# Optimization experiments

Hardware: AMD Instinct MI355X
Metric: run time of the kernel (lower is better)

Reference implementation:

```python
import jax, jax.numpy as jnp
import numpy as np

N_NODES = 50000


def gcn_conv(x, src, dst, inv_sqrt_deg, W):
    # GCNConv: h = x @ W^T, then out[i] = sum_{j->i} norm_ji * h[j]
    h = x @ W.T                                   # [N, out]
    norm = inv_sqrt_deg[src] * inv_sqrt_deg[dst]  # [E]
    msg = h[src] * norm[:, None]                  # [E, out] gather
    return jax.ops.segment_sum(msg, dst, num_segments=N_NODES)  # scatter-add


def setup_inputs() -> dict:
    key = jax.random.key(0)
    k1, k2, k3, k4, k5 = jax.random.split(key, 5)
    x = jax.random.normal(k1, (N_NODES, 500), dtype=jnp.float32)
    edge_index = jax.random.randint(k2, (2, 1600000), 0, N_NODES, dtype=jnp.int64)
    W1 = jax.random.normal(k3, (128, 500), dtype=jnp.float32) * 0.04
    W2 = jax.random.normal(k4, (128, 128), dtype=jnp.float32) * 0.08
    Wlin = jax.random.normal(k5, (16, 128), dtype=jnp.float32) * 0.08
    return {"x": x, "edge_index": edge_index, "W1": W1, "W2": W2, "Wlin": Wlin}


def reference(x, edge_index, W1, W2, Wlin):
    # add self-loops (GCNConv default)
    loop = jnp.arange(N_NODES, dtype=edge_index.dtype)
    src = jnp.concatenate([edge_index[0], loop])
    dst = jnp.concatenate([edge_index[1], loop])
    # symmetric normalization: deg counted on destination (in-degree incl. self-loop)
    deg = jax.ops.segment_sum(jnp.ones_like(src, dtype=x.dtype), dst, num_segments=N_NODES)
    inv_sqrt_deg = jnp.where(deg > 0, jax.lax.rsqrt(deg), 0.0)

    h = gcn_conv(x, src, dst, inv_sqrt_deg, W1)
    h = jax.nn.relu(h)
    h = gcn_conv(h, src, dst, inv_sqrt_deg, W2)
    # dropout is identity in eval mode (training=False reference)
    return h @ Wlin.T  # [N, num_classes]
```

## Files before the change

kernel.cpp:

```cpp
#include <hip/hip_runtime.h>

#define N_NODES 50000
#define F_IN 500
#define F_HID 128
#define F_OUT 16
#define NSCAN_BLKS ((N_NODES + 255) / 256)


__device__ __forceinline__ unsigned bf16_pack2(float a, float b) {
    unsigned ua = __float_as_uint(a);
    unsigned ub = __float_as_uint(b);
    ua = (ua + 0x7fffu + ((ua >> 16) & 1u)) >> 16;
    ub = (ub + 0x7fffu + ((ub >> 16) & 1u)) >> 16;
    return ua | (ub << 16);
}
__device__ __forceinline__ float bf_lo(unsigned v) { return __uint_as_float(v << 16); }
__device__ __forceinline__ float bf_hi(unsigned v) { return __uint_as_float(v & 0xffff0000u); }

__device__ __forceinline__ unsigned bf16_rtne(float a) {
    unsigned u = __float_as_uint(a);
    return (u + 0x7fffu + ((u >> 16) & 1u)) >> 16;
}


__global__ void k_hist_rank(const int* __restrict__ dst, int* __restrict__ hist,
                            int* __restrict__ rank, int E) {
    int e = blockIdx.x * 256 + threadIdx.x;
    if (e < E) rank[e] = atomicAdd(&hist[dst[e]], 1);
}

__global__ __launch_bounds__(256) void k_scan_local(const int* __restrict__ hist,
                                                    int* __restrict__ rowptr,
                                                    int* __restrict__ blksum) {
    __shared__ int s[256];
    const int tid = threadIdx.x;
    const int i = blockIdx.x * 256 + tid;
    int v = (i < N_NODES) ? hist[i] : 0;
    s[tid] = v;
    __syncthreads();
#pragma unroll
    for (int ofs = 1; ofs < 256; ofs <<= 1) {
        int t = (tid >= ofs) ? s[tid - ofs] : 0;
        __syncthreads();
        if (tid >= ofs) s[tid] += t;
        __syncthreads();
    }
    if (i < N_NODES) rowptr[i] = s[tid] - v;
    if (tid == 255) blksum[blockIdx.x] = s[255];
}

__global__ __launch_bounds__(256) void k_scan_blk(int* __restrict__ blksum) {
    __shared__ int s[256];
    const int tid = threadIdx.x;
    int v = (tid < NSCAN_BLKS) ? blksum[tid] : 0;
    s[tid] = v;
    __syncthreads();
#pragma unroll
    for (int ofs = 1; ofs < 256; ofs <<= 1) {
        int t = (tid >= ofs) ? s[tid - ofs] : 0;
        __syncthreads();
        if (tid >= ofs) s[tid] += t;
        __syncthreads();
    }
    if (tid < NSCAN_BLKS) blksum[tid] = s[tid] - v;
}

__global__ void k_finalize(const int* __restrict__ hist, int* __restrict__ rowptr,
                           const int* __restrict__ blksum, float* __restrict__ isd, int E) {
    int i = blockIdx.x * 256 + threadIdx.x;
    if (i < N_NODES) {
        rowptr[i] = rowptr[i] + blksum[i >> 8];
        isd[i] = rsqrtf((float)(hist[i] + 1));
    }
    if (i == 0) rowptr[N_NODES] = E;
}

__global__ void k_reorder(const int* __restrict__ src, const int* __restrict__ dst,
                          const int* __restrict__ rank, const int* __restrict__ rowptr,
                          int* __restrict__ csr_src, int E) {
    int e = blockIdx.x * 256 + threadIdx.x;
    if (e >= E) return;
    csr_src[rowptr[dst[e]] + rank[e]] = src[e];
}


__global__ void k_wc(const float* __restrict__ W2, const float* __restrict__ Wlin,
                     float* __restrict__ Wc) {
    const int c = blockIdx.x;
    const int j = threadIdx.x;
    const float* wl = Wlin + c * 128;
    float acc = 0.f;
#pragma unroll 4
    for (int k = 0; k < 128; ++k) acc += wl[k] * W2[k * 128 + j];
    Wc[c * 128 + j] = acc;
}


__global__ __launch_bounds__(256) void k_w1pack(const float* __restrict__ W1,
                                                ushort* __restrict__ wpk) {
    int t = blockIdx.x * 256 + threadIdx.x;
    if (t >= 8192) return;
    const int lane = t & 63;
    const int fkt = t >> 6;
    const int f = fkt & 7;
    const int kt = fkt >> 3;
    const int n = (f << 4) + (lane & 15);
    const int kb = (kt << 5) + ((lane >> 4) << 3);
    ushort h8[8], l8[8];
#pragma unroll
    for (int j = 0; j < 8; ++j) {
        const int k = kb + j;
        float v = (k < F_IN) ? W1[n * F_IN + k] : 0.f;
        unsigned h = bf16_rtne(v);
        float fh = __uint_as_float(h << 16);
        unsigned l = bf16_rtne(v - fh);
        h8[j] = (ushort)h;
        l8[j] = (ushort)l;
    }
    const size_t base = ((size_t)fkt << 10);
    *(uint4*)(wpk + base + (lane << 3))       = *(const uint4*)h8;
    *(uint4*)(wpk + base + 512 + (lane << 3)) = *(const uint4*)l8;
}


typedef __attribute__((ext_vector_type(8))) short s16x8;
typedef __attribute__((ext_vector_type(4))) float f32x4;

typedef const __attribute__((address_space(1))) unsigned u32_glb;
typedef __attribute__((address_space(3))) unsigned u32_lds;

__device__ __forceinline__ void glds16(const void* g, void* l) {
    __builtin_amdgcn_global_load_lds((u32_glb*)g, (u32_lds*)l, 16, 0, 0);
}

__global__ __launch_bounds__(256) void gemm1_mfma5(const float* __restrict__ A,
                                                   const ushort* __restrict__ wpk,
                                                   const float* __restrict__ isd,
                                                   unsigned* __restrict__ hb, int M) {
    __shared__ __align__(16) ushort Bs[2][8192];

    const int tid = threadIdx.x;
    const int lane = tid & 63;
    const int wave = tid >> 6;
    const int jcol = lane & 15;
    const int kgrp = lane >> 4;
    const int klo  = kgrp << 3;

    const int m0  = blockIdx.x * 64 + wave * 16;
    const int arw = m0 + jcol;
    const float* arow = A + (size_t)((arw < M) ? arw : (M - 1)) * F_IN;

#define ISSUE_TILE(KT, B)                                                        \
    {                                                                            \
        const ushort* tb_ = wpk + ((size_t)(KT) << 13);                          \
        _Pragma("unroll") for (int c_ = 0; c_ < 4; ++c_) {                       \
            glds16(tb_ + ((c_ * 256 + wave * 64 + lane) << 3),                   \
                   &Bs[B][(c_ * 256 + wave * 64) << 3]);                         \
        }                                                                        \
    }

    const float4 zf4 = make_float4(0.f, 0.f, 0.f, 0.f);
    float4 ca0 = zf4, ca1 = zf4;

    ISSUE_TILE(0, 0);
    ca0 = *(const float4*)(arow + klo);
    ca1 = *(const float4*)(arow + klo + 4);
    __syncthreads();

    f32x4 acc[8] = {};

    for (int kt = 0; kt < 16; ++kt) {
        const int cb = kt & 1, nb = (kt + 1) & 1;

        float4 na0 = zf4, na1 = zf4;
        if (kt + 1 < 16) {
            ISSUE_TILE(kt + 1, nb);
            const int k = ((kt + 1) << 5) + klo;
            if (k + 8 <= F_IN) {
                na0 = *(const float4*)(arow + k);
                na1 = *(const float4*)(arow + k + 4);
            } else {
                float tmp[8];
#pragma unroll
                for (int i = 0; i < 8; ++i) tmp[i] = (k + i < F_IN) ? arow[k + i] : 0.f;
                na0 = make_float4(tmp[0], tmp[1], tmp[2], tmp[3]);
                na1 = make_float4(tmp[4], tmp[5], tmp[6], tmp[7]);
            }
        }

        const float av[8] = {ca0.x, ca0.y, ca0.z, ca0.w, ca1.x, ca1.y, ca1.z, ca1.w};
        s16x8 ahi, alo;
#pragma unroll
        for (int i = 0; i < 8; ++i) {
            unsigned h = bf16_rtne(av[i]);
            float fh = __uint_as_float(h << 16);
            unsigned l = bf16_rtne(av[i] - fh);
            ahi[i] = (short)h;
            alo[i] = (short)l;
        }

#pragma unroll
        for (int f = 0; f < 8; ++f) {
            const s16x8 bh = *(const s16x8*)&Bs[cb][(f << 10) + (lane << 3)];
            const s16x8 bl = *(const s16x8*)&Bs[cb][(f << 10) + 512 + (lane << 3)];
            acc[f] = __builtin_amdgcn_mfma_f32_16x16x32_bf16(ahi, bh, acc[f], 0, 0, 0);
            acc[f] = __builtin_amdgcn_mfma_f32_16x16x32_bf16(alo, bh, acc[f], 0, 0, 0);
            acc[f] = __builtin_amdgcn_mfma_f32_16x16x32_bf16(ahi, bl, acc[f], 0, 0, 0);
        }

        ca0 = na0;
        ca1 = na1;
        __syncthreads();
    }
#undef ISSUE_TILE

    const int orow = m0 + (kgrp << 2);
    float sr[4];
#pragma unroll
    for (int r = 0; r < 4; ++r) {
        const int m = orow + r;
        sr[r] = (m < M) ? isd[m] : 0.f;
    }
#pragma unroll
    for (int f = 0; f < 8; ++f) {
#pragma unroll
        for (int r = 0; r < 4; ++r) {
            float v = acc[f][r] * sr[r];
            float o = __shfl_xor(v, 1, 64);
            if (!(jcol & 1)) {
                const int m = orow + r;
                if (m < M)
                    hb[(size_t)m * 64 + (f << 3) + (jcol >> 1)] = bf16_pack2(v, o);
            }
        }
    }
}


__device__ __forceinline__ void gather_range(const unsigned* __restrict__ hh,
                                             const int* __restrict__ csr_src,
                                             int lane, int e, int end,
                                             float& accx, float& accy) {
    int s[8], t[8];
    bool have = (e + 8 <= end);
    if (have) {
#pragma unroll
        for (int i = 0; i < 8; ++i) s[i] = csr_src[e + i];
    }
    while (have) {
        unsigned v[8];
#pragma unroll
        for (int i = 0; i < 8; ++i) v[i] = hh[(size_t)s[i] * 64 + lane];
        const int ne = e + 8;
        const bool nhave = (ne + 8 <= end);
        if (nhave) {
#pragma unroll
            for (int i = 0; i < 8; ++i) t[i] = csr_src[ne + i];
        }
#pragma unroll
        for (int i = 0; i < 8; ++i) {
            accx += bf_lo(v[i]);
            accy += bf_hi(v[i]);
        }
#pragma unroll
        for (int i = 0; i < 8; ++i) s[i] = t[i];
        e = ne;
        have = nhave;
    }
    if (e < end) {
        const int last = end - 1;
        int ss[8];
        unsigned vv[8];
#pragma unroll
        for (int i = 0; i < 8; ++i) ss[i] = csr_src[(e + i < end) ? e + i : last];
#pragma unroll
        for (int i = 0; i < 8; ++i) vv[i] = hh[(size_t)ss[i] * 64 + lane];
#pragma unroll
        for (int i = 0; i < 8; ++i) {
            if (e + i < end) {
                accx += bf_lo(vv[i]);
                accy += bf_hi(vv[i]);
            }
        }
    }
}

__global__ __launch_bounds__(256) void k_gather_fused2(const unsigned* __restrict__ hh,
                                                       const int* __restrict__ rowptr,
                                                       const int* __restrict__ csr_src,
                                                       const float* __restrict__ isd,
                                                       const float* __restrict__ Wc,
                                                       float* __restrict__ z) {
    __shared__ float2 part[2][64];
    const int tid = threadIdx.x;
    const int lane = tid & 63;
    const int waveid = tid >> 6;
    const int slot = waveid >> 1;
    const int half = waveid & 1;
    const int node = (blockIdx.x << 1) + slot;

    const int e0 = rowptr[node], e1 = rowptr[node + 1];
    const int mid = e0 + ((e1 - e0) >> 1);

    float accx = 0.f, accy = 0.f;
    if (half == 0) {
        const unsigned a = hh[(size_t)node * 64 + lane];
        accx = bf_lo(a);
        accy = bf_hi(a);
        gather_range(hh, csr_src, lane, e0, mid, accx, accy);
    } else {
        gather_range(hh, csr_src, lane, mid, e1, accx, accy);
        part[slot][lane] = make_float2(accx, accy);
    }
    __syncthreads();
    if (half == 1) return;

    const float2 pb = part[slot][lane];
    accx += pb.x;
    accy += pb.y;

    const float si = isd[node];
    const float rx = fmaxf(accx * si, 0.f), ry = fmaxf(accy * si, 0.f);
    float p[16];
#pragma unroll
    for (int c = 0; c < 16; ++c) {
        const float2 wc = *(const float2*)(Wc + c * 128 + (lane << 1));
        p[c] = rx * wc.x + ry * wc.y;
    }
#pragma unroll
    for (int m = 1; m < 64; m <<= 1) {
#pragma unroll
        for (int c = 0; c < 16; ++c) p[c] += __shfl_xor(p[c], m, 64);
    }
    if (lane == 0) {
        float* zr = z + (size_t)node * 16;
        *(float4*)(zr + 0)  = make_float4(si * p[0],  si * p[1],  si * p[2],  si * p[3]);
        *(float4*)(zr + 4)  = make_float4(si * p[4],  si * p[5],  si * p[6],  si * p[7]);
        *(float4*)(zr + 8)  = make_float4(si * p[8],  si * p[9],  si * p[10], si * p[11]);
        *(float4*)(zr + 12) = make_float4(si * p[12], si * p[13], si * p[14], si * p[15]);
    }
}


__global__ __launch_bounds__(256) void k_gather16(const float4* __restrict__ z4,
                                                  const int* __restrict__ rowptr,
                                                  const int* __restrict__ csr_src,
                                                  const float* __restrict__ isd,
                                                  float4* __restrict__ out4) {
    int t = blockIdx.x * 256 + threadIdx.x;
    int n = t >> 2, q = t & 3;
    if (n >= N_NODES) return;
    const float si = isd[n];
    float4 acc = z4[(size_t)n * 4 + q];
    int e = rowptr[n];
    const int end = rowptr[n + 1];
    for (; e + 4 <= end; e += 4) {
        int s0 = csr_src[e],     s1 = csr_src[e + 1];
        int s2 = csr_src[e + 2], s3 = csr_src[e + 3];
        float4 v0 = z4[(size_t)s0 * 4 + q];
        float4 v1 = z4[(size_t)s1 * 4 + q];
        float4 v2 = z4[(size_t)s2 * 4 + q];
        float4 v3 = z4[(size_t)s3 * 4 + q];
        acc.x += v0.x + v1.x + v2.x + v3.x;
        acc.y += v0.y + v1.y + v2.y + v3.y;
        acc.z += v0.z + v1.z + v2.z + v3.z;
        acc.w += v0.w + v1.w + v2.w + v3.w;
    }
    for (; e < end; ++e) {
        int s = csr_src[e];
        float4 v = z4[(size_t)s * 4 + q];
        acc.x += v.x; acc.y += v.y; acc.z += v.z; acc.w += v.w;
    }
    acc.x *= si; acc.y *= si; acc.z *= si; acc.w *= si;
    out4[(size_t)n * 4 + q] = acc;
}


__global__ void k_deg_init(float* __restrict__ deg) {
    int i = blockIdx.x * 256 + threadIdx.x;
    if (i < N_NODES) deg[i] = 1.0f;
}
__global__ void k_deg_count(const int* __restrict__ dst, float* __restrict__ deg, int E) {
    int e = blockIdx.x * 256 + threadIdx.x;
    if (e < E) atomicAdd(&deg[dst[e]], 1.0f);
}
__global__ void k_rsqrt(float* __restrict__ deg) {
    int i = blockIdx.x * 256 + threadIdx.x;
    if (i < N_NODES) deg[i] = rsqrtf(deg[i]);
}
__global__ void k_agg_init(const float4* __restrict__ h, const float* __restrict__ isd,
                           float4* __restrict__ agg) {
    int t = blockIdx.x * 256 + threadIdx.x;
    if (t < N_NODES * (F_HID / 4)) {
        int row = t >> 5;
        float s = isd[row];
        s = s * s;
        float4 v = h[t];
        v.x *= s; v.y *= s; v.z *= s; v.w *= s;
        agg[t] = v;
    }
}
__global__ void k_scatter(const float4* __restrict__ h, const int* __restrict__ src,
                          const int* __restrict__ dst, const float* __restrict__ isd,
                          float* __restrict__ agg, int E) {
    int t = blockIdx.x * 256 + threadIdx.x;
    int e = t >> 5, q = t & 31;
    if (e >= E) return;
    int s = src[e], d = dst[e];
    float norm = isd[s] * isd[d];
    float4 v = h[(long long)s * 32 + q];
    float* out = agg + (long long)d * F_HID + q * 4;
    atomicAdd(out + 0, v.x * norm);
    atomicAdd(out + 1, v.y * norm);
    atomicAdd(out + 2, v.z * norm);
    atomicAdd(out + 3, v.w * norm);
}
template <int BM, int BN, int BK, int TM, int TN, bool RELU_A>
__global__ __launch_bounds__(256) void gemm_nt(const float* __restrict__ A,
                                               const float* __restrict__ B,
                                               float* __restrict__ C,
                                               int M, int N, int K) {
    __shared__ float As[BK][BM + 1];
    __shared__ float Bs[BK][BN + 1];
    const int tid = threadIdx.x;
    const int NTX = BN / TN;
    const int tx = tid % NTX;
    const int ty = tid / NTX;
    const int m0 = blockIdx.x * BM;
    const int n0 = blockIdx.y * BN;
    float acc[TM][TN] = {};
    for (int k0 = 0; k0 < K; k0 += BK) {
        for (int idx = tid; idx < BM * BK; idx += 256) {
            int m = idx / BK, k = idx % BK;
            int gm = m0 + m;
            float v = (gm < M) ? A[(long long)gm * K + k0 + k] : 0.0f;
            if (RELU_A) v = fmaxf(v, 0.0f);
            As[k][m] = v;
        }
        for (int idx = tid; idx < BN * BK; idx += 256) {
            int n = idx / BK, k = idx % BK;
            int gn = n0 + n;
            Bs[k][n] = (gn < N) ? B[(long long)gn * K + k0 + k] : 0.0f;
        }
        __syncthreads();
        for (int k = 0; k < BK; ++k) {
            float a[TM], b[TN];
#pragma unroll
            for (int r = 0; r < TM; ++r) a[r] = As[k][ty * TM + r];
#pragma unroll
            for (int c = 0; c < TN; ++c) b[c] = Bs[k][c * NTX + tx];
#pragma unroll
            for (int r = 0; r < TM; ++r)
#pragma unroll
                for (int c = 0; c < TN; ++c) acc[r][c] += a[r] * b[c];
        }
        __syncthreads();
    }
#pragma unroll
    for (int r = 0; r < TM; ++r) {
        int gm = m0 + ty * TM + r;
        if (gm >= M) continue;
#pragma unroll
        for (int c = 0; c < TN; ++c) {
            int gn = n0 + c * NTX + tx;
            if (gn < N) C[(long long)gm * N + gn] = acc[r][c];
        }
    }
}
__global__ __launch_bounds__(256) void gemm_lin(const float* __restrict__ A,
                                                const float* __restrict__ W,
                                                float* __restrict__ C, int M) {
    __shared__ float Ws[16][129];
    __shared__ float As[16][129];
    const int tid = threadIdx.x;
    for (int idx = tid; idx < 16 * 128; idx += 256) Ws[idx >> 7][idx & 127] = W[idx];
    const int m0 = blockIdx.x * 16;
    for (int idx = tid; idx < 16 * 128; idx += 256) {
        int r = idx >> 7, k = idx & 127;
        int gm = m0 + r;
        As[r][k] = (gm < M) ? A[(long long)gm * 128 + k] : 0.0f;
    }
    __syncthreads();
    const int tc = tid & 15, tr = tid >> 4;
    float s = 0.f;
#pragma unroll 8
    for (int k = 0; k < 128; ++k) s += As[tr][k] * Ws[tc][k];
    int gm = m0 + tr;
    if (gm < M) C[gm * 16 + tc] = s;
}


static inline size_t align256(size_t x) { return (x + 255) & ~(size_t)255; }

extern "C" void kernel_launch(void* const* d_in, const int* in_sizes, int n_in,
                              void* d_out, int out_size, void* d_ws, size_t ws_size,
                              hipStream_t stream) {
    const float* x    = (const float*)d_in[0];
    const int*   ei   = (const int*)d_in[1];
    const float* W1   = (const float*)d_in[2];
    const float* W2   = (const float*)d_in[3];
    const float* Wlin = (const float*)d_in[4];
    float* out = (float*)d_out;

    const int E = in_sizes[1] / 2;
    const int* src = ei;
    const int* dst = ei + E;

    char* ws = (char*)d_ws;
    size_t off = 0;
    float* isd  = (float*)(ws + off); off += align256((size_t)N_NODES * 4);
    float* Wc   = (float*)(ws + off); off += align256(16 * 128 * 4);
    float* bufA = (float*)(ws + off); off += align256((size_t)N_NODES * F_HID * 4);
    float* bufB = (float*)(ws + off); off += align256((size_t)N_NODES * F_HID * 4);
    int*   hist    = (int*)(ws + off); off += align256((size_t)N_NODES * 4);
    int*   rowptr  = (int*)(ws + off); off += align256(((size_t)N_NODES + 1) * 4);
    int*   blksum  = (int*)(ws + off); off += align256(256 * 4);
    int*   csr_src = (int*)(ws + off); off += align256((size_t)E * 4);
    int*   rank    = (int*)(ws + off); off += align256((size_t)E * 4);
    ushort* wpk    = (ushort*)(ws + off); off += align256((size_t)16 * 8192 * 2);
    const bool use_csr = (off <= ws_size);

    const int nblk_nodes = NSCAN_BLKS;
    const int nblk_edges = (E + 255) / 256;
    const int mtiles = (N_NODES + 63) / 64;

    if (use_csr) {
        unsigned* hb = (unsigned*)bufB;
        float*    z  = bufA;

        hipMemsetAsync(hist, 0, (size_t)N_NODES * 4, stream);
        k_hist_rank<<<nblk_edges, 256, 0, stream>>>(dst, hist, rank, E);
        k_scan_local<<<nblk_nodes, 256, 0, stream>>>(hist, rowptr, blksum);
        k_scan_blk<<<1, 256, 0, stream>>>(blksum);
        k_finalize<<<nblk_nodes, 256, 0, stream>>>(hist, rowptr, blksum, isd, E);
        k_reorder<<<nblk_edges, 256, 0, stream>>>(src, dst, rank, rowptr, csr_src, E);
        k_wc<<<16, 128, 0, stream>>>(W2, Wlin, Wc);
        k_w1pack<<<32, 256, 0, stream>>>(W1, wpk);
        gemm1_mfma5<<<mtiles, 256, 0, stream>>>(x, wpk, isd, hb, N_NODES);
        k_gather_fused2<<<N_NODES / 2, 256, 0, stream>>>(
            hb, rowptr, csr_src, isd, Wc, z);
        k_gather16<<<(N_NODES * 4 + 255) / 256, 256, 0, stream>>>(
            (const float4*)z, rowptr, csr_src, isd, (float4*)out);
    } else {
        const int nblk_feat = (N_NODES * (F_HID / 4) + 255) / 256;
        const int nblk_scatter = (int)(((long long)E * 32 + 255) / 256);
        k_deg_init<<<(N_NODES + 255) / 256, 256, 0, stream>>>(isd);
        k_deg_count<<<nblk_edges, 256, 0, stream>>>(dst, isd, E);
        k_rsqrt<<<(N_NODES + 255) / 256, 256, 0, stream>>>(isd);
        gemm_nt<64, 128, 20, 4, 8, false>
            <<<dim3(mtiles, 1), 256, 0, stream>>>(x, W1, bufA, N_NODES, F_HID, F_IN);
        k_agg_init<<<nblk_feat, 256, 0, stream>>>((const float4*)bufA, isd, (float4*)bufB);
        k_scatter<<<nblk_scatter, 256, 0, stream>>>((const float4*)bufA, src, dst, isd, bufB, E);
        gemm_nt<64, 128, 16, 4, 8, true>
            <<<dim3(mtiles, 1), 256, 0, stream>>>(bufB, W2, bufA, N_NODES, F_HID, F_HID);
        k_agg_init<<<nblk_feat, 256, 0, stream>>>((const float4*)bufA, isd, (float4*)bufB);
        k_scatter<<<nblk_scatter, 256, 0, stream>>>((const float4*)bufA, src, dst, isd, bufB, E);
        gemm_lin<<<(N_NODES + 15) / 16, 256, 0, stream>>>(bufB, Wlin, out, N_NODES);
    }
}
```

Baseline: 405.1 us.

## Gather two edges per wave with 8-byte loads and split output projection across waves

The layer-2 gather now has each half-wave read a different neighbour row using 8-byte uint2 loads, so one wave covers two edges per load instruction. The half-wave partial sums are combined with a cross-half shuffle. The final 16-column projection, which the first wave used to do alone, is split so each of the two waves computes 8 output columns with float4 weight loads and a shorter shuffle reduction. The aim is fewer memory instructions and less serial reduction work, at the cost of extra shuffles and fewer independent loads in flight per lane.

```diff
diff --git a/kernel.cpp b/kernel.cpp
--- a/kernel.cpp
+++ b/kernel.cpp
@@ -237,49 +237,53 @@
 }
 
 
-__device__ __forceinline__ void gather_range(const unsigned* __restrict__ hh,
+__device__ __forceinline__ void gather_pairs(const unsigned* __restrict__ hh,
                                              const int* __restrict__ csr_src,
-                                             int lane, int e, int end,
-                                             float& accx, float& accy) {
-    int s[8], t[8];
+                                             int lane, int e, int end, float4& acc) {
+    const int half32 = lane >> 5;
+    const int c2 = (lane & 31) << 1;
+    int s[4], t[4];
     bool have = (e + 8 <= end);
     if (have) {
 #pragma unroll
-        for (int i = 0; i < 8; ++i) s[i] = csr_src[e + i];
+        for (int i = 0; i < 4; ++i) s[i] = csr_src[e + 2 * i + half32];
     }
     while (have) {
-        unsigned v[8];
-#pragma unroll
-        for (int i = 0; i < 8; ++i) v[i] = hh[(size_t)s[i] * 64 + lane];
+        uint2 v[4];
+#pragma unroll
+        for (int i = 0; i < 4; ++i) v[i] = *(const uint2*)(hh + (size_t)s[i] * 64 + c2);
         const int ne = e + 8;
         const bool nhave = (ne + 8 <= end);
         if (nhave) {
 #pragma unroll
-            for (int i = 0; i < 8; ++i) t[i] = csr_src[ne + i];
-        }
-#pragma unroll
-        for (int i = 0; i < 8; ++i) {
-            accx += bf_lo(v[i]);
-            accy += bf_hi(v[i]);
-        }
-#pragma unroll
-        for (int i = 0; i < 8; ++i) s[i] = t[i];
+            for (int i = 0; i < 4; ++i) t[i] = csr_src[ne + 2 * i + half32];
+        }
+#pragma unroll
+        for (int i = 0; i < 4; ++i) {
+            acc.x += bf_lo(v[i].x); acc.y += bf_hi(v[i].x);
+            acc.z += bf_lo(v[i].y); acc.w += bf_hi(v[i].y);
+        }
+#pragma unroll
+        for (int i = 0; i < 4; ++i) s[i] = t[i];
         e = ne;
         have = nhave;
     }
     if (e < end) {
         const int last = end - 1;
-        int ss[8];
-        unsigned vv[8];
-#pragma unroll
-        for (int i = 0; i < 8; ++i) ss[i] = csr_src[(e + i < end) ? e + i : last];
-#pragma unroll
-        for (int i = 0; i < 8; ++i) vv[i] = hh[(size_t)ss[i] * 64 + lane];
-#pragma unroll
-        for (int i = 0; i < 8; ++i) {
-            if (e + i < end) {
-                accx += bf_lo(vv[i]);
-                accy += bf_hi(vv[i]);
+        int ss[4];
+        uint2 vv[4];
+#pragma unroll
+        for (int i = 0; i < 4; ++i) {
+            const int idx = e + 2 * i + half32;
+            ss[i] = csr_src[(idx <= last) ? idx : last];
+        }
+#pragma unroll
+        for (int i = 0; i < 4; ++i) vv[i] = *(const uint2*)(hh + (size_t)ss[i] * 64 + c2);
+#pragma unroll
+        for (int i = 0; i < 4; ++i) {
+            if (e + 2 * i + half32 <= last) {
+                acc.x += bf_lo(vv[i].x); acc.y += bf_hi(vv[i].x);
+                acc.z += bf_lo(vv[i].y); acc.w += bf_hi(vv[i].y);
             }
         }
     }
@@ -291,7 +295,7 @@
                                                        const float* __restrict__ isd,
                                                        const float* __restrict__ Wc,
                                                        float* __restrict__ z) {
-    __shared__ float2 part[2][64];
+    __shared__ float4 part[2][2][64];
     const int tid = threadIdx.x;
     const int lane = tid & 63;
     const int waveid = tid >> 6;
@@ -301,43 +305,50 @@
 
     const int e0 = rowptr[node], e1 = rowptr[node + 1];
     const int mid = e0 + ((e1 - e0) >> 1);
-
-    float accx = 0.f, accy = 0.f;
+    const int c2 = (lane & 31) << 1;
+
+    float4 acc = make_float4(0.f, 0.f, 0.f, 0.f);
     if (half == 0) {
-        const unsigned a = hh[(size_t)node * 64 + lane];
-        accx = bf_lo(a);
-        accy = bf_hi(a);
-        gather_range(hh, csr_src, lane, e0, mid, accx, accy);
+        const uint2 a = *(const uint2*)(hh + (size_t)node * 64 + c2);
+        if (lane < 32) {
+            acc.x = bf_lo(a.x); acc.y = bf_hi(a.x);
+            acc.z = bf_lo(a.y); acc.w = bf_hi(a.y);
+        }
+        gather_pairs(hh, csr_src, lane, e0, mid, acc);
     } else {
-        gather_range(hh, csr_src, lane, mid, e1, accx, accy);
-        part[slot][lane] = make_float2(accx, accy);
-    }
+        gather_pairs(hh, csr_src, lane, mid, e1, acc);
+    }
+    part[slot][half][lane] = acc;
     __syncthreads();
-    if (half == 1) return;
-
-    const float2 pb = part[slot][lane];
-    accx += pb.x;
-    accy += pb.y;
+
+    const float4 pb = part[slot][half ^ 1][lane];
+    acc.x += pb.x; acc.y += pb.y; acc.z += pb.z; acc.w += pb.w;
+
+    acc.x += __shfl_xor(acc.x, 32, 64);
+    acc.y += __shfl_xor(acc.y, 32, 64);
+    acc.z += __shfl_xor(acc.z, 32, 64);
+    acc.w += __shfl_xor(acc.w, 32, 64);
 
     const float si = isd[node];
-    const float rx = fmaxf(accx * si, 0.f), ry = fmaxf(accy * si, 0.f);
-    float p[16];
-#pragma unroll
-    for (int c = 0; c < 16; ++c) {
-        const float2 wc = *(const float2*)(Wc + c * 128 + (lane << 1));
-        p[c] = rx * wc.x + ry * wc.y;
-    }
-#pragma unroll
-    for (int m = 1; m < 64; m <<= 1) {
-#pragma unroll
-        for (int c = 0; c < 16; ++c) p[c] += __shfl_xor(p[c], m, 64);
+    const float r0 = fmaxf(acc.x * si, 0.f), r1 = fmaxf(acc.y * si, 0.f);
+    const float r2 = fmaxf(acc.z * si, 0.f), r3 = fmaxf(acc.w * si, 0.f);
+
+    float p[8];
+    const float* wcb = Wc + (half << 3) * 128 + ((lane & 31) << 2);
+#pragma unroll
+    for (int c = 0; c < 8; ++c) {
+        const float4 wc = *(const float4*)(wcb + c * 128);
+        p[c] = r0 * wc.x + r1 * wc.y + r2 * wc.z + r3 * wc.w;
+    }
+#pragma unroll
+    for (int m = 1; m < 32; m <<= 1) {
+#pragma unroll
+        for (int c = 0; c < 8; ++c) p[c] += __shfl_xor(p[c], m, 64);
     }
     if (lane == 0) {
-        float* zr = z + (size_t)node * 16;
-        *(float4*)(zr + 0)  = make_float4(si * p[0],  si * p[1],  si * p[2],  si * p[3]);
-        *(float4*)(zr + 4)  = make_float4(si * p[4],  si * p[5],  si * p[6],  si * p[7]);
-        *(float4*)(zr + 8)  = make_float4(si * p[8],  si * p[9],  si * p[10], si * p[11]);
-        *(float4*)(zr + 12) = make_float4(si * p[12], si * p[13], si * p[14], si * p[15]);
+        float* zr = z + (size_t)node * 16 + (half << 3);
+        *(float4*)(zr + 0) = make_float4(si * p[0], si * p[1], si * p[2], si * p[3]);
+        *(float4*)(zr + 4) = make_float4(si * p[4], si * p[5], si * p[6], si * p[7]);
     }
 }
 
```

Result: no change. 411.3 us (+1.6%).
